# Performance work log

Measured on AMD Instinct MI355X. Metric: run time of the kernel, lower is better.

Reference implementation:

```python
import jax, jax.numpy as jnp
import numpy as np

N_QUBITS = 2
N_LAYERS = 2
EPS = 1e-12  # tf.math.l2_normalize epsilon


def _apply_rx(state, theta, wire):
    """Apply RX(theta) to `wire` of a batched 2-qubit state.
    state: [B,2,2] complex64 (axis1 = qubit0, axis2 = qubit1); theta: [B] float.
    RX(t) = [[cos(t/2), -i sin(t/2)], [-i sin(t/2), cos(t/2)]]
    """
    c = jnp.cos(theta * 0.5)[:, None].astype(state.dtype)
    s = (-1j * jnp.sin(theta * 0.5))[:, None].astype(state.dtype)
    if wire == 0:
        a, b = state[:, 0, :], state[:, 1, :]
        return jnp.stack([c * a + s * b, s * a + c * b], axis=1)
    else:
        a, b = state[:, :, 0], state[:, :, 1]
        return jnp.stack([c * a + s * b, s * a + c * b], axis=2)


def _cnot01(state):
    # CNOT control=0, target=1: flip qubit1 where qubit0 == 1
    return jnp.stack([state[:, 0, :], state[:, 1, ::-1]], axis=1)


def _circuit(angles, weights_q):
    """angles: [B,2] embedding angles; weights_q: [L,2]. Returns [B,2] <Z_i>."""
    B = angles.shape[0]
    state = jnp.zeros((B, 2, 2), dtype=jnp.complex64).at[:, 0, 0].set(1.0)
    # AngleEmbedding (RX rotations, one per wire)
    state = _apply_rx(state, angles[:, 0], 0)
    state = _apply_rx(state, angles[:, 1], 1)
    # BasicEntanglerLayers: RX per wire then single CNOT(0,1) for 2 wires
    for l in range(weights_q.shape[0]):
        state = _apply_rx(state, jnp.broadcast_to(weights_q[l, 0], (B,)), 0)
        state = _apply_rx(state, jnp.broadcast_to(weights_q[l, 1], (B,)), 1)
        state = _cnot01(state)
    probs = (state * jnp.conj(state)).real  # [B,2,2]
    z0 = probs[:, 0, :].sum(-1) - probs[:, 1, :].sum(-1)
    z1 = probs[:, :, 0].sum(-1) - probs[:, :, 1].sum(-1)
    return jnp.stack([z0, z1], axis=-1).astype(jnp.float32)


def setup_inputs() -> dict:
    key = jax.random.key(0)
    k1, k2, k3, k4 = jax.random.split(key, 4)
    B, D = 65536, 1024
    return {
        "x": jax.random.normal(k1, (B, D), dtype=jnp.float32),
        "dense_w": jax.random.normal(k2, (D, N_QUBITS), dtype=jnp.float32) * 0.05,
        "dense_b": jax.random.normal(k3, (N_QUBITS,), dtype=jnp.float32) * 0.05,
        "weights_q": jax.random.normal(k4, (N_LAYERS, N_QUBITS), dtype=jnp.float32) * 0.05,
    }


def reference(x, dense_w, dense_b, weights_q):
    h = x @ dense_w + dense_b  # [B,2]
    # tf.math.l2_normalize(h, axis=-1)
    h = h * jax.lax.rsqrt(jnp.maximum(jnp.sum(h * h, axis=-1, keepdims=True), EPS))
    return _circuit(h, weights_q)  # [B,2]
```

## Files before the change

kernel.cpp:

```cpp
#include <hip/hip_runtime.h>


#define WAVES_PER_BLOCK 4
#define ROWS_PER_WAVE   8
#define ROWS_PER_BLOCK  (WAVES_PER_BLOCK * ROWS_PER_WAVE)

__device__ __forceinline__ float2 run_circuit(
    float h0, float h1,
    float c00, float s00, float c01, float s01,
    float c10, float s10, float c11, float s11)
{
    float inv = rsqrtf(fmaxf(h0 * h0 + h1 * h1, 1e-12f));
    float t0 = 0.5f * h0 * inv;
    float t1 = 0.5f * h1 * inv;
    float s0 = __sinf(t0), c0 = __cosf(t0);
    float s1 = __sinf(t1), c1 = __cosf(t1);

    float r00 = c0 * c1,   i00 = 0.0f;
    float r01 = 0.0f,      i01 = -c0 * s1;
    float r10 = 0.0f,      i10 = -s0 * c1;
    float r11 = -s0 * s1,  i11 = 0.0f;

    float ar, ai, br, bi, tr, ti;

#define RX_W0(c, s)                                                  \
    ar = r00; ai = i00; br = r10; bi = i10;                          \
    r00 = c * ar + s * bi; i00 = c * ai - s * br;                    \
    r10 = s * ai + c * br; i10 = c * bi - s * ar;                    \
    ar = r01; ai = i01; br = r11; bi = i11;                          \
    r01 = c * ar + s * bi; i01 = c * ai - s * br;                    \
    r11 = s * ai + c * br; i11 = c * bi - s * ar;

#define RX_W1(c, s)                                                  \
    ar = r00; ai = i00; br = r01; bi = i01;                          \
    r00 = c * ar + s * bi; i00 = c * ai - s * br;                    \
    r01 = s * ai + c * br; i01 = c * bi - s * ar;                    \
    ar = r10; ai = i10; br = r11; bi = i11;                          \
    r10 = c * ar + s * bi; i10 = c * ai - s * br;                    \
    r11 = s * ai + c * br; i11 = c * bi - s * ar;

#define CNOT01()                                                     \
    tr = r10; ti = i10; r10 = r11; i10 = i11; r11 = tr; i11 = ti;

    RX_W0(c00, s00)
    RX_W1(c01, s01)
    CNOT01()
    RX_W0(c10, s10)
    RX_W1(c11, s11)
    CNOT01()

#undef RX_W0
#undef RX_W1
#undef CNOT01

    float p00 = r00 * r00 + i00 * i00;
    float p01 = r01 * r01 + i01 * i01;
    float p10 = r10 * r10 + i10 * i10;
    float p11 = r11 * r11 + i11 * i11;

    float2 z;
    z.x = (p00 + p01) - (p10 + p11);
    z.y = (p00 + p10) - (p01 + p11);
    return z;
}

__global__ __launch_bounds__(256) void qlayer_kernel(
    const float* __restrict__ x,
    const float* __restrict__ w,
    const float* __restrict__ bias,
    const float* __restrict__ wq,
    float* __restrict__ out,
    int B)
{
    const int lane = threadIdx.x & 63;
    const int wave = threadIdx.x >> 6;
    const int rowBase = (blockIdx.x * WAVES_PER_BLOCK + wave) * ROWS_PER_WAVE;
    if (rowBase >= B) return;

    const float4* __restrict__ w4 = (const float4*)w;
    float4 wA0, wB0, wA1, wB1, wA2, wB2, wA3, wB3;
    wA0 = w4[2 * (lane +   0)]; wB0 = w4[2 * (lane +   0) + 1];
    wA1 = w4[2 * (lane +  64)]; wB1 = w4[2 * (lane +  64) + 1];
    wA2 = w4[2 * (lane + 128)]; wB2 = w4[2 * (lane + 128) + 1];
    wA3 = w4[2 * (lane + 192)]; wB3 = w4[2 * (lane + 192) + 1];

    const float b0 = bias[0], b1 = bias[1];

    const float c00 = __cosf(0.5f * wq[0]), s00 = __sinf(0.5f * wq[0]);
    const float c01 = __cosf(0.5f * wq[1]), s01 = __sinf(0.5f * wq[1]);
    const float c10 = __cosf(0.5f * wq[2]), s10 = __sinf(0.5f * wq[2]);
    const float c11 = __cosf(0.5f * wq[3]), s11 = __sinf(0.5f * wq[3]);

    float2* __restrict__ out2 = (float2*)out;

#pragma unroll
    for (int r = 0; r < ROWS_PER_WAVE; r += 4) {
        const int row0 = rowBase + r;

        const float4* __restrict__ xA = (const float4*)x + (size_t)(row0 + 0) * 256;
        const float4* __restrict__ xB = (const float4*)x + (size_t)(row0 + 1) * 256;
        const float4* __restrict__ xC = (const float4*)x + (size_t)(row0 + 2) * 256;
        const float4* __restrict__ xD = (const float4*)x + (size_t)(row0 + 3) * 256;

        float a0 = 0.f, a1 = 0.f, b0s = 0.f, b1s = 0.f;
        float e0 = 0.f, e1 = 0.f, d0 = 0.f, d1 = 0.f;

#define DOT(v, wA, wB, acc0, acc1)                                   \
        acc0 = fmaf(v.x, wA.x, acc0); acc1 = fmaf(v.x, wA.y, acc1);  \
        acc0 = fmaf(v.y, wA.z, acc0); acc1 = fmaf(v.y, wA.w, acc1);  \
        acc0 = fmaf(v.z, wB.x, acc0); acc1 = fmaf(v.z, wB.y, acc1);  \
        acc0 = fmaf(v.w, wB.z, acc0); acc1 = fmaf(v.w, wB.w, acc1);

#define STEP(j, wA, wB)                                              \
        {                                                            \
            float4 va = xA[lane + 64 * j];                           \
            float4 vb = xB[lane + 64 * j];                           \
            float4 vc = xC[lane + 64 * j];                           \
            float4 vd = xD[lane + 64 * j];                           \
            DOT(va, wA, wB, a0, a1)                                  \
            DOT(vb, wA, wB, b0s, b1s)                                \
            DOT(vc, wA, wB, e0, e1)                                  \
            DOT(vd, wA, wB, d0, d1)                                  \
        }

        STEP(0, wA0, wB0)
        STEP(1, wA1, wB1)
        STEP(2, wA2, wB2)
        STEP(3, wA3, wB3)

#undef STEP
#undef DOT

#pragma unroll
        for (int off = 32; off >= 1; off >>= 1) {
            a0  += __shfl_xor(a0, off, 64);
            a1  += __shfl_xor(a1, off, 64);
            b0s += __shfl_xor(b0s, off, 64);
            b1s += __shfl_xor(b1s, off, 64);
            e0  += __shfl_xor(e0, off, 64);
            e1  += __shfl_xor(e1, off, 64);
            d0  += __shfl_xor(d0, off, 64);
            d1  += __shfl_xor(d1, off, 64);
        }

        float2 zA = run_circuit(a0 + b0, a1 + b1, c00, s00, c01, s01, c10, s10, c11, s11);
        float2 zB = run_circuit(b0s + b0, b1s + b1, c00, s00, c01, s01, c10, s10, c11, s11);
        float2 zC = run_circuit(e0 + b0, e1 + b1, c00, s00, c01, s01, c10, s10, c11, s11);
        float2 zD = run_circuit(d0 + b0, d1 + b1, c00, s00, c01, s01, c10, s10, c11, s11);

        if (lane == 0) {
            out2[row0 + 0] = zA;
            out2[row0 + 1] = zB;
            out2[row0 + 2] = zC;
            out2[row0 + 3] = zD;
        }
    }
}

extern "C" void kernel_launch(void* const* d_in, const int* in_sizes, int n_in,
                              void* d_out, int out_size, void* d_ws, size_t ws_size,
                              hipStream_t stream) {
    const float* x    = (const float*)d_in[0];
    const float* w    = (const float*)d_in[1];
    const float* bias = (const float*)d_in[2];
    const float* wq   = (const float*)d_in[3];
    float* out = (float*)d_out;

    const int B = in_sizes[0] / 1024;
    const int grid = (B + ROWS_PER_BLOCK - 1) / ROWS_PER_BLOCK;
    qlayer_kernel<<<grid, 256, 0, stream>>>(x, w, bias, wq, out, B);
}
```

Measured before the change: 357.1 us.

## Split each wave into half-waves per row and double rows per wave

```diff
diff --git a/kernel.cpp b/kernel.cpp
--- a/kernel.cpp
+++ b/kernel.cpp
@@ -2,7 +2,7 @@
 
 
 #define WAVES_PER_BLOCK 4
-#define ROWS_PER_WAVE   8
+#define ROWS_PER_WAVE   16
 #define ROWS_PER_BLOCK  (WAVES_PER_BLOCK * ROWS_PER_WAVE)
 
 __device__ __forceinline__ float2 run_circuit(
@@ -73,16 +73,20 @@
     int B)
 {
     const int lane = threadIdx.x & 63;
+    const int li   = lane & 31;
+    const int half = lane >> 5;
     const int wave = threadIdx.x >> 6;
     const int rowBase = (blockIdx.x * WAVES_PER_BLOCK + wave) * ROWS_PER_WAVE;
     if (rowBase >= B) return;
 
     const float4* __restrict__ w4 = (const float4*)w;
-    float4 wA0, wB0, wA1, wB1, wA2, wB2, wA3, wB3;
-    wA0 = w4[2 * (lane +   0)]; wB0 = w4[2 * (lane +   0) + 1];
-    wA1 = w4[2 * (lane +  64)]; wB1 = w4[2 * (lane +  64) + 1];
-    wA2 = w4[2 * (lane + 128)]; wB2 = w4[2 * (lane + 128) + 1];
-    wA3 = w4[2 * (lane + 192)]; wB3 = w4[2 * (lane + 192) + 1];
+    float4 wA[8], wB[8];
+#pragma unroll
+    for (int j = 0; j < 8; ++j) {
+        const int f = li + 32 * j;
+        wA[j] = w4[2 * f];
+        wB[j] = w4[2 * f + 1];
+    }
 
     const float b0 = bias[0], b1 = bias[1];
 
@@ -94,65 +98,46 @@
     float2* __restrict__ out2 = (float2*)out;
 
 #pragma unroll
-    for (int r = 0; r < ROWS_PER_WAVE; r += 4) {
-        const int row0 = rowBase + r;
+    for (int p = 0; p < ROWS_PER_WAVE / 4; ++p) {
+        const int r0 = rowBase + 4 * p;
+        if (r0 + 3 >= B + 0 && r0 >= B) break;
 
-        const float4* __restrict__ xA = (const float4*)x + (size_t)(row0 + 0) * 256;
-        const float4* __restrict__ xB = (const float4*)x + (size_t)(row0 + 1) * 256;
-        const float4* __restrict__ xC = (const float4*)x + (size_t)(row0 + 2) * 256;
-        const float4* __restrict__ xD = (const float4*)x + (size_t)(row0 + 3) * 256;
+        const float4* __restrict__ x0 = (const float4*)x + (size_t)(r0 + half) * 256;
+        const float4* __restrict__ x1 = (const float4*)x + (size_t)(r0 + 2 + half) * 256;
 
-        float a0 = 0.f, a1 = 0.f, b0s = 0.f, b1s = 0.f;
-        float e0 = 0.f, e1 = 0.f, d0 = 0.f, d1 = 0.f;
+        float4 v0[8], v1[8];
+#pragma unroll
+        for (int j = 0; j < 8; ++j) v0[j] = x0[li + 32 * j];
+#pragma unroll
+        for (int j = 0; j < 8; ++j) v1[j] = x1[li + 32 * j];
 
-#define DOT(v, wA, wB, acc0, acc1)                                   \
-        acc0 = fmaf(v.x, wA.x, acc0); acc1 = fmaf(v.x, wA.y, acc1);  \
-        acc0 = fmaf(v.y, wA.z, acc0); acc1 = fmaf(v.y, wA.w, acc1);  \
-        acc0 = fmaf(v.z, wB.x, acc0); acc1 = fmaf(v.z, wB.y, acc1);  \
-        acc0 = fmaf(v.w, wB.z, acc0); acc1 = fmaf(v.w, wB.w, acc1);
-
-#define STEP(j, wA, wB)                                              \
-        {                                                            \
-            float4 va = xA[lane + 64 * j];                           \
-            float4 vb = xB[lane + 64 * j];                           \
-            float4 vc = xC[lane + 64 * j];                           \
-            float4 vd = xD[lane + 64 * j];                           \
-            DOT(va, wA, wB, a0, a1)                                  \
-            DOT(vb, wA, wB, b0s, b1s)                                \
-            DOT(vc, wA, wB, e0, e1)                                  \
-            DOT(vd, wA, wB, d0, d1)                                  \
+        float a0 = 0.f, a1 = 0.f, e0 = 0.f, e1 = 0.f;
+#pragma unroll
+        for (int j = 0; j < 8; ++j) {
+            a0 = fmaf(v0[j].x, wA[j].x, a0); a1 = fmaf(v0[j].x, wA[j].y, a1);
+            a0 = fmaf(v0[j].y, wA[j].z, a0); a1 = fmaf(v0[j].y, wA[j].w, a1);
+            a0 = fmaf(v0[j].z, wB[j].x, a0); a1 = fmaf(v0[j].z, wB[j].y, a1);
+            a0 = fmaf(v0[j].w, wB[j].z, a0); a1 = fmaf(v0[j].w, wB[j].w, a1);
+            e0 = fmaf(v1[j].x, wA[j].x, e0); e1 = fmaf(v1[j].x, wA[j].y, e1);
+            e0 = fmaf(v1[j].y, wA[j].z, e0); e1 = fmaf(v1[j].y, wA[j].w, e1);
+            e0 = fmaf(v1[j].z, wB[j].x, e0); e1 = fmaf(v1[j].z, wB[j].y, e1);
+            e0 = fmaf(v1[j].w, wB[j].z, e0); e1 = fmaf(v1[j].w, wB[j].w, e1);
         }
 
-        STEP(0, wA0, wB0)
-        STEP(1, wA1, wB1)
-        STEP(2, wA2, wB2)
-        STEP(3, wA3, wB3)
-
-#undef STEP
-#undef DOT
-
 #pragma unroll
-        for (int off = 32; off >= 1; off >>= 1) {
-            a0  += __shfl_xor(a0, off, 64);
-            a1  += __shfl_xor(a1, off, 64);
-            b0s += __shfl_xor(b0s, off, 64);
-            b1s += __shfl_xor(b1s, off, 64);
-            e0  += __shfl_xor(e0, off, 64);
-            e1  += __shfl_xor(e1, off, 64);
-            d0  += __shfl_xor(d0, off, 64);
-            d1  += __shfl_xor(d1, off, 64);
+        for (int off = 16; off >= 1; off >>= 1) {
+            a0 += __shfl_xor(a0, off, 64);
+            a1 += __shfl_xor(a1, off, 64);
+            e0 += __shfl_xor(e0, off, 64);
+            e1 += __shfl_xor(e1, off, 64);
         }
 
-        float2 zA = run_circuit(a0 + b0, a1 + b1, c00, s00, c01, s01, c10, s10, c11, s11);
-        float2 zB = run_circuit(b0s + b0, b1s + b1, c00, s00, c01, s01, c10, s10, c11, s11);
-        float2 zC = run_circuit(e0 + b0, e1 + b1, c00, s00, c01, s01, c10, s10, c11, s11);
-        float2 zD = run_circuit(d0 + b0, d1 + b1, c00, s00, c01, s01, c10, s10, c11, s11);
+        float2 z0 = run_circuit(a0 + b0, a1 + b1, c00, s00, c01, s01, c10, s10, c11, s11);
+        float2 z1 = run_circuit(e0 + b0, e1 + b1, c00, s00, c01, s01, c10, s10, c11, s11);
 
-        if (lane == 0) {
-            out2[row0 + 0] = zA;
-            out2[row0 + 1] = zB;
-            out2[row0 + 2] = zC;
-            out2[row0 + 3] = zD;
+        if (li == 0) {
+            out2[r0 + half]     = z0;
+            out2[r0 + 2 + half] = z1;
         }
     }
 }
```

Measured after the change: 361.0 us. About the same (+1.1%).
